# Optimization experiments

Measured on AMD Instinct MI355X. Metric: run time of the kernel, lower is better.

## Reference

```python
import jax, jax.numpy as jnp
import numpy as np

NUM_GRAPHS = 128
NUM_LAYERS = 3
BN_EPS = 1e-5


def setup_inputs() -> dict:
    key = jax.random.key(0)
    ks = jax.random.split(key, 8)
    N, E, D, C = 100000, 1250000, 64, 10
    x = jax.random.normal(ks[0], (N, D), dtype=jnp.float32)
    edge_index = jax.random.randint(ks[1], (2, E), 0, N, dtype=jnp.int64)
    batch = jnp.sort(jax.random.randint(ks[2], (N,), 0, NUM_GRAPHS, dtype=jnp.int64))
    W_rel = jax.random.normal(ks[3], (NUM_LAYERS, D, D), dtype=jnp.float32) * (1.0 / np.sqrt(D))
    b_rel = jax.random.normal(ks[4], (NUM_LAYERS, D), dtype=jnp.float32) * 0.01
    W_root = jax.random.normal(ks[5], (NUM_LAYERS, D, D), dtype=jnp.float32) * (1.0 / np.sqrt(D))
    gamma = jnp.ones((NUM_LAYERS, D), dtype=jnp.float32)
    beta = jnp.zeros((NUM_LAYERS, D), dtype=jnp.float32)
    W_cls = jax.random.normal(ks[6], (D, C), dtype=jnp.float32) * (1.0 / np.sqrt(D))
    b_cls = jnp.zeros((C,), dtype=jnp.float32)
    return {"x": x, "edge_index": edge_index, "batch": batch,
            "W_rel": W_rel, "b_rel": b_rel, "W_root": W_root,
            "gamma": gamma, "beta": beta, "W_cls": W_cls, "b_cls": b_cls}


def reference(x, edge_index, batch, W_rel, b_rel, W_root, gamma, beta, W_cls, b_cls):
    N = x.shape[0]
    src, dst = edge_index[0], edge_index[1]
    for l in range(NUM_LAYERS):
        # GraphConv: lin_rel(sum-aggregated neighbor feats) + lin_root(x)
        msg = jax.ops.segment_sum(x[src], dst, num_segments=N)  # [N, D]
        h = msg @ W_rel[l] + b_rel[l] + x @ W_root[l]
        # BatchNorm1d over nodes (batch statistics, training-mode math)
        mean = jnp.mean(h, axis=0)
        var = jnp.var(h, axis=0)
        h = (h - mean) * jax.lax.rsqrt(var + BN_EPS) * gamma[l] + beta[l]
        x = jax.nn.relu(h)  # dropout is identity at inference
    # global_mean_pool: segment mean over graph ids
    counts = jax.ops.segment_sum(jnp.ones((N,), dtype=x.dtype), batch, num_segments=NUM_GRAPHS)
    pooled = jax.ops.segment_sum(x, batch, num_segments=NUM_GRAPHS)
    pooled = pooled / jnp.maximum(counts, 1.0)[:, None]  # [G, D]
    return pooled @ W_cls + b_cls
```

## Files before the change

### kernel.cpp

```cpp
#include <hip/hip_runtime.h>

#define D 64
#define NGRAPH 128
#define NCLS 10
#define BN_EPS 1e-5f
#define BUCK_SZ 512
#define EPB 8192

typedef __attribute__((ext_vector_type(8))) __bf16 bf16x8;
typedef __attribute__((ext_vector_type(4))) float floatx4;

union BF8 { bf16x8 v; ushort u[8]; };

__device__ __forceinline__ unsigned f2bf_rne(float f) {
  unsigned u = __float_as_uint(f);
  return (u + 0x7FFFu + ((u >> 16) & 1u)) >> 16;
}
__device__ __forceinline__ unsigned pack2bf(float a, float b) {
  return f2bf_rne(a) | (f2bf_rne(b) << 16);
}
__device__ __forceinline__ float4 bf4_to_f4(uint2 u) {
  float4 r;
  r.x = __uint_as_float(u.x << 16);
  r.y = __uint_as_float(u.x & 0xFFFF0000u);
  r.z = __uint_as_float(u.y << 16);
  r.w = __uint_as_float(u.y & 0xFFFF0000u);
  return r;
}

__device__ __forceinline__ void bn_sc_sh(
    const float* __restrict__ stats, const float* __restrict__ gamma,
    const float* __restrict__ beta, float invN, int f, float* sc, float* sh) {
  float mean = stats[f] * invN;
  float var = stats[D + f] * invN - mean * mean;
  float s = gamma[f] * rsqrtf(var + BN_EPS);
  *sc = s;
  *sh = beta[f] - mean * s;
}

__device__ __forceinline__ void split8(float4 a, float4 b,
                                       bf16x8* hi, bf16x8* lo) {
  float f[8] = {a.x, a.y, a.z, a.w, b.x, b.y, b.z, b.w};
  BF8 H, L;
#pragma unroll
  for (int t = 0; t < 8; t++) {
    unsigned u = __float_as_uint(f[t]);
    H.u[t] = (ushort)(u >> 16);
    float hf = __uint_as_float(u & 0xFFFF0000u);
    float lf = f[t] - hf;
    L.u[t] = (ushort)(__float_as_uint(lf) >> 16);
  }
  *hi = H.v;
  *lo = L.v;
}

__global__ __launch_bounds__(256) void bucket_scatter_kernel(
    const int* __restrict__ ei, int* __restrict__ gcnt, int* __restrict__ pk,
    int E, int capB, int nbuck) {
  __shared__ int hist[256];
  __shared__ int base[256];
  int t = threadIdx.x;
  int e0 = blockIdx.x * EPB;
  int e1 = min(e0 + EPB, E);
  hist[t] = 0;
  __syncthreads();
  for (int e = e0 + t; e < e1; e += 256)
    atomicAdd(&hist[ei[E + e] >> 9], 1);
  __syncthreads();
  int h = hist[t];
  if (t < nbuck && h > 0) base[t] = atomicAdd(&gcnt[t], h);
  hist[t] = 0;
  __syncthreads();
  for (int e = e0 + t; e < e1; e += 256) {
    int s = ei[e];
    int d = ei[E + e];
    int b = d >> 9;
    int pos = base[b] + atomicAdd(&hist[b], 1);
    if (pos < capB) pk[(size_t)b * capB + pos] = (s << 9) | (d & (BUCK_SZ - 1));
  }
}

__global__ void bucket_scan_kernel(const int* __restrict__ gcnt,
                                   int* __restrict__ bstart,
                                   int* __restrict__ row_start,
                                   int nbuck, int N, int capB) {
  __shared__ int s[256];
  int t = threadIdx.x;
  int v = (t < nbuck) ? min(gcnt[t], capB) : 0;
  s[t] = v;
  __syncthreads();
  for (int off = 1; off < 256; off <<= 1) {
    int add = (t >= off) ? s[t - off] : 0;
    __syncthreads();
    s[t] += add;
    __syncthreads();
  }
  if (t < nbuck) bstart[t] = s[t] - v;
  if (t == 0) {
    bstart[nbuck] = s[255];
    row_start[N] = s[255];
  }
}

__global__ __launch_bounds__(256) void bucket_place_kernel(
    const int* __restrict__ pk, const int* __restrict__ gcnt,
    const int* __restrict__ bstart, int* __restrict__ row_start,
    int* __restrict__ csr_src, int N, int capB) {
  __shared__ int hist[BUCK_SZ];
  __shared__ int scn[256];
  __shared__ int cur[BUCK_SZ];
  int b = blockIdx.x;
  int t = threadIdx.x;
  hist[t] = 0;
  hist[t + 256] = 0;
  int cnt = min(gcnt[b], capB);
  const int* seg = pk + (size_t)b * capB;
  __syncthreads();
  for (int e = t; e < cnt; e += 256)
    atomicAdd(&hist[seg[e] & (BUCK_SZ - 1)], 1);
  __syncthreads();
  scn[t] = hist[2 * t] + hist[2 * t + 1];
  __syncthreads();
  for (int off = 1; off < 256; off <<= 1) {
    int add = (t >= off) ? scn[t - off] : 0;
    __syncthreads();
    scn[t] += add;
    __syncthreads();
  }
  int base = bstart[b];
  int ex = (t == 0) ? 0 : scn[t - 1];
  int c0 = base + ex;
  int c1 = c0 + hist[2 * t];
  cur[2 * t] = c0;
  cur[2 * t + 1] = c1;
  int dst0 = b * BUCK_SZ + 2 * t;
  if (dst0 < N) row_start[dst0] = c0;
  if (dst0 + 1 < N) row_start[dst0 + 1] = c1;
  __syncthreads();
  for (int e = t; e < cnt; e += 256) {
    int p = seg[e];
    int slot = atomicAdd(&cur[p & (BUCK_SZ - 1)], 1);
    csr_src[slot] = p >> 9;
  }
}

__global__ __launch_bounds__(256) void wsplit_kernel(
    const float* __restrict__ Wrel, const float* __restrict__ Wroot,
    ushort* __restrict__ wfrag) {
  int l = blockIdx.x;
  const float* Wr = Wrel + l * 4096;
  const float* Wo = Wroot + l * 4096;
  ushort* base = wfrag + l * 16384;
  for (int slot = threadIdx.x; slot < 1024; slot += 256) {
    int kt = slot >> 8, nt = (slot >> 6) & 3, lane = slot & 63;
    int quad = lane >> 4, c = lane & 15;
    ushort* ph = base + (((kt * 4 + nt) * 2 + 0) * 64 + lane) * 8;
    ushort* pl = base + (((kt * 4 + nt) * 2 + 1) * 64 + lane) * 8;
#pragma unroll
    for (int j = 0; j < 8; j++) {
      int k = kt * 32 + quad * 8 + j;
      int n = nt * 16 + c;
      float w = (k < 64) ? Wr[k * 64 + n] : Wo[(k - 64) * 64 + n];
      unsigned u = __float_as_uint(w);
      ph[j] = (ushort)(u >> 16);
      float lf = w - __uint_as_float(u & 0xFFFF0000u);
      pl[j] = (ushort)(__float_as_uint(lf) >> 16);
    }
  }
}

__global__ __launch_bounds__(256) void xprep_kernel(
    const float* __restrict__ x, ushort* __restrict__ xbf, int n) {
  int base = (blockIdx.x * 256 + threadIdx.x) * 8;
  if (base >= n) return;
  float4 a = *(const float4*)(x + base);
  float4 b = *(const float4*)(x + base + 4);
  uint4 o;
  o.x = pack2bf(a.x, a.y);
  o.y = pack2bf(a.z, a.w);
  o.z = pack2bf(b.x, b.y);
  o.w = pack2bf(b.z, b.w);
  *(uint4*)(xbf + base) = o;
}

__global__ __launch_bounds__(256) void gather_kernel(
    const ushort* __restrict__ xbf, const int* __restrict__ csr_src,
    const int* __restrict__ row_start, const float* __restrict__ stats_prev,
    const float* __restrict__ gamma, const float* __restrict__ beta,
    float invN, int apply, float* __restrict__ msg, int N) {
  int i = blockIdx.x * 4 + (threadIdx.x >> 6);
  int lane = threadIdx.x & 63;
  int q = lane >> 4;
  int f = (lane & 15) << 2;
  if (i >= N) return;
  int e0 = row_start[i], e1 = row_start[i + 1];
  int cnt = e1 - e0;
  int myidx = csr_src[e0 + lane];
  float4 acc = {0.f, 0.f, 0.f, 0.f};
  float4 sc, sh;
  if (apply) {
    bn_sc_sh(stats_prev, gamma, beta, invN, f + 0, &sc.x, &sh.x);
    bn_sc_sh(stats_prev, gamma, beta, invN, f + 1, &sc.y, &sh.y);
    bn_sc_sh(stats_prev, gamma, beta, invN, f + 2, &sc.z, &sh.z);
    bn_sc_sh(stats_prev, gamma, beta, invN, f + 3, &sc.w, &sh.w);
  }

  int cnt64 = min(cnt, 64);
  for (int base = 0; base < cnt64; base += 16) {
    int j0 = base + q;
    int s0 = __shfl(myidx, j0);
    int s1 = __shfl(myidx, j0 + 4);
    int s2 = __shfl(myidx, j0 + 8);
    int s3 = __shfl(myidx, j0 + 12);
    float m0 = (j0 < cnt) ? 1.f : 0.f;
    float m1 = (j0 + 4 < cnt) ? 1.f : 0.f;
    float m2 = (j0 + 8 < cnt) ? 1.f : 0.f;
    float m3 = (j0 + 12 < cnt) ? 1.f : 0.f;
    s0 = (j0 < cnt) ? s0 : 0;
    s1 = (j0 + 4 < cnt) ? s1 : 0;
    s2 = (j0 + 8 < cnt) ? s2 : 0;
    s3 = (j0 + 12 < cnt) ? s3 : 0;
    float4 v0 = bf4_to_f4(*(const uint2*)(xbf + (size_t)s0 * D + f));
    float4 v1 = bf4_to_f4(*(const uint2*)(xbf + (size_t)s1 * D + f));
    float4 v2 = bf4_to_f4(*(const uint2*)(xbf + (size_t)s2 * D + f));
    float4 v3 = bf4_to_f4(*(const uint2*)(xbf + (size_t)s3 * D + f));
    if (apply) {
      acc.x += m0 * fmaxf(v0.x * sc.x + sh.x, 0.f) + m1 * fmaxf(v1.x * sc.x + sh.x, 0.f)
             + m2 * fmaxf(v2.x * sc.x + sh.x, 0.f) + m3 * fmaxf(v3.x * sc.x + sh.x, 0.f);
      acc.y += m0 * fmaxf(v0.y * sc.y + sh.y, 0.f) + m1 * fmaxf(v1.y * sc.y + sh.y, 0.f)
             + m2 * fmaxf(v2.y * sc.y + sh.y, 0.f) + m3 * fmaxf(v3.y * sc.y + sh.y, 0.f);
      acc.z += m0 * fmaxf(v0.z * sc.z + sh.z, 0.f) + m1 * fmaxf(v1.z * sc.z + sh.z, 0.f)
             + m2 * fmaxf(v2.z * sc.z + sh.z, 0.f) + m3 * fmaxf(v3.z * sc.z + sh.z, 0.f);
      acc.w += m0 * fmaxf(v0.w * sc.w + sh.w, 0.f) + m1 * fmaxf(v1.w * sc.w + sh.w, 0.f)
             + m2 * fmaxf(v2.w * sc.w + sh.w, 0.f) + m3 * fmaxf(v3.w * sc.w + sh.w, 0.f);
    } else {
      acc.x += m0 * v0.x + m1 * v1.x + m2 * v2.x + m3 * v3.x;
      acc.y += m0 * v0.y + m1 * v1.y + m2 * v2.y + m3 * v3.y;
      acc.z += m0 * v0.z + m1 * v1.z + m2 * v2.z + m3 * v3.z;
      acc.w += m0 * v0.w + m1 * v1.w + m2 * v2.w + m3 * v3.w;
    }
  }

  for (int e = e0 + 64 + q; e < e1; e += 4) {
    float4 v = bf4_to_f4(*(const uint2*)(xbf + (size_t)csr_src[e] * D + f));
    if (apply) {
      acc.x += fmaxf(v.x * sc.x + sh.x, 0.f);
      acc.y += fmaxf(v.y * sc.y + sh.y, 0.f);
      acc.z += fmaxf(v.z * sc.z + sh.z, 0.f);
      acc.w += fmaxf(v.w * sc.w + sh.w, 0.f);
    } else {
      acc.x += v.x; acc.y += v.y; acc.z += v.z; acc.w += v.w;
    }
  }

  acc.x += __shfl_xor(acc.x, 16); acc.x += __shfl_xor(acc.x, 32);
  acc.y += __shfl_xor(acc.y, 16); acc.y += __shfl_xor(acc.y, 32);
  acc.z += __shfl_xor(acc.z, 16); acc.z += __shfl_xor(acc.z, 32);
  acc.w += __shfl_xor(acc.w, 16); acc.w += __shfl_xor(acc.w, 32);
  if (q == 0) *(float4*)(msg + (size_t)i * D + f) = acc;
}

__global__ __launch_bounds__(256, 1) void mm_mfma_kernel(
    const float* msg, const float* xf32, const ushort* xbfin,
    const ushort* __restrict__ wfrag, const float* __restrict__ brel,
    const float* __restrict__ stats_prev, const float* __restrict__ gamma,
    const float* __restrict__ beta, float invN, int apply,
    float* h, ushort* hbf, int wh, int wbf, float* __restrict__ stats_cur,
    int N, int ntiles, int nwaves) {
  __shared__ float ssum[4][64];
  __shared__ float ssq[4][64];
  int tid = threadIdx.x;
  int lane = tid & 63;
  int wvid = tid >> 6;
  int wv = (blockIdx.x * 256 + tid) >> 6;
  int quad = lane >> 4;
  int lo4 = lane & 15;

  bf16x8 bf[4][4][2];
#pragma unroll
  for (int kt = 0; kt < 4; kt++)
#pragma unroll
    for (int nt = 0; nt < 4; nt++)
#pragma unroll
      for (int s = 0; s < 2; s++)
        bf[kt][nt][s] =
            *(const bf16x8*)(wfrag + (((kt * 4 + nt) * 2 + s) * 64 + lane) * 8);

  float bias[4];
#pragma unroll
  for (int nt = 0; nt < 4; nt++) bias[nt] = brel[nt * 16 + lo4];

  float scx[2][8], shx[2][8];
  if (apply) {
#pragma unroll
    for (int hh = 0; hh < 2; hh++)
#pragma unroll
      for (int jj = 0; jj < 8; jj++) {
        int f = hh * 32 + quad * 8 + jj;
        bn_sc_sh(stats_prev, gamma, beta, invN, f, &scx[hh][jj], &shx[hh][jj]);
      }
  }

  float psum[4] = {0.f, 0.f, 0.f, 0.f};
  float psq[4] = {0.f, 0.f, 0.f, 0.f};

  for (int t = wv; t < ntiles; t += nwaves) {
    int i0 = t * 16;
    int row = i0 + lo4;
    if (row >= N) row = N - 1;
    bf16x8 ahi[4], alo[4];
#pragma unroll
    for (int kt = 0; kt < 4; kt++) {
      float4 a, b;
      if (kt < 2) {
        const float* p = msg + (size_t)row * D + (kt & 1) * 32 + quad * 8;
        a = *(const float4*)p;
        b = *(const float4*)(p + 4);
      } else if (apply) {
        const ushort* p = xbfin + (size_t)row * D + (kt & 1) * 32 + quad * 8;
        uint4 u = *(const uint4*)p;
        uint2 ulo = {u.x, u.y}, uhi = {u.z, u.w};
        a = bf4_to_f4(ulo);
        b = bf4_to_f4(uhi);
        int hh = kt - 2;
        a.x = fmaxf(a.x * scx[hh][0] + shx[hh][0], 0.f);
        a.y = fmaxf(a.y * scx[hh][1] + shx[hh][1], 0.f);
        a.z = fmaxf(a.z * scx[hh][2] + shx[hh][2], 0.f);
        a.w = fmaxf(a.w * scx[hh][3] + shx[hh][3], 0.f);
        b.x = fmaxf(b.x * scx[hh][4] + shx[hh][4], 0.f);
        b.y = fmaxf(b.y * scx[hh][5] + shx[hh][5], 0.f);
        b.z = fmaxf(b.z * scx[hh][6] + shx[hh][6], 0.f);
        b.w = fmaxf(b.w * scx[hh][7] + shx[hh][7], 0.f);
      } else {
        const float* p = xf32 + (size_t)row * D + (kt & 1) * 32 + quad * 8;
        a = *(const float4*)p;
        b = *(const float4*)(p + 4);
      }
      split8(a, b, &ahi[kt], &alo[kt]);
    }
#pragma unroll
    for (int nt = 0; nt < 4; nt++) {
      floatx4 acc = {bias[nt], bias[nt], bias[nt], bias[nt]};
#pragma unroll
      for (int kt = 0; kt < 4; kt++) {
        acc = __builtin_amdgcn_mfma_f32_16x16x32_bf16(ahi[kt], bf[kt][nt][0],
                                                      acc, 0, 0, 0);
        acc = __builtin_amdgcn_mfma_f32_16x16x32_bf16(ahi[kt], bf[kt][nt][1],
                                                      acc, 0, 0, 0);
        acc = __builtin_amdgcn_mfma_f32_16x16x32_bf16(alo[kt], bf[kt][nt][0],
                                                      acc, 0, 0, 0);
      }
#pragma unroll
      for (int r = 0; r < 4; r++) {
        int grow = i0 + quad * 4 + r;
        if (grow < N) {
          float v = acc[r];
          size_t idx = (size_t)grow * D + nt * 16 + lo4;
          if (wh) h[idx] = v;
          if (wbf) hbf[idx] = (ushort)f2bf_rne(v);
          psum[nt] += v;
          psq[nt] += v * v;
        }
      }
    }
  }

#pragma unroll
  for (int nt = 0; nt < 4; nt++) {
    float s = psum[nt], q = psq[nt];
    s += __shfl_xor(s, 16); s += __shfl_xor(s, 32);
    q += __shfl_xor(q, 16); q += __shfl_xor(q, 32);
    if (lane < 16) { ssum[wvid][nt * 16 + lane] = s; ssq[wvid][nt * 16 + lane] = q; }
  }
  __syncthreads();
  if (tid < 64) {
    atomicAdd(&stats_cur[tid],
              ssum[0][tid] + ssum[1][tid] + ssum[2][tid] + ssum[3][tid]);
  } else if (tid < 128) {
    int c = tid - 64;
    atomicAdd(&stats_cur[D + c],
              ssq[0][c] + ssq[1][c] + ssq[2][c] + ssq[3][c]);
  }
}

__global__ __launch_bounds__(256) void norm_relu_pool_kernel(
    const float* __restrict__ h, const float* __restrict__ stats,
    const float* __restrict__ gamma, const float* __restrict__ beta,
    float invN, const int* __restrict__ batch, float* __restrict__ pooled,
    int N) {
  int j = threadIdx.x & 63;
  int q = threadIdx.x >> 6;
  int i0 = blockIdx.x * 256;
  float sc, sh;
  bn_sc_sh(stats, gamma, beta, invN, j, &sc, &sh);
  int curg = -1;
  float acc = 0.f;
  for (int r = q; r < 256; r += 4) {
    int i = i0 + r;
    if (i >= N) break;
    int b = batch[i];
    float v = fmaxf(h[(size_t)i * D + j] * sc + sh, 0.f);
    if (b != curg) {
      if (curg >= 0) atomicAdd(&pooled[curg * D + j], acc);
      curg = b;
      acc = v;
    } else {
      acc += v;
    }
  }
  if (curg >= 0) atomicAdd(&pooled[curg * D + j], acc);
}

__global__ void cls_kernel(const float* __restrict__ pooled,
                           const int* __restrict__ batch,
                           const float* __restrict__ Wcls,
                           const float* __restrict__ bcls,
                           float* __restrict__ out, int N) {
  int tid = blockIdx.x * blockDim.x + threadIdx.x;
  if (tid >= NGRAPH * NCLS) return;
  int g = tid / NCLS, c = tid % NCLS;
  int lo = 0, hi = N;
  while (lo < hi) { int m = (lo + hi) >> 1; if (batch[m] < g) lo = m + 1; else hi = m; }
  int start = lo;
  lo = 0; hi = N;
  while (lo < hi) { int m = (lo + hi) >> 1; if (batch[m] <= g) lo = m + 1; else hi = m; }
  float inv = 1.f / fmaxf((float)(lo - start), 1.f);
  float acc = bcls[c];
#pragma unroll 8
  for (int k = 0; k < D; k++) acc += pooled[g * D + k] * inv * Wcls[k * NCLS + c];
  out[g * NCLS + c] = acc;
}

extern "C" void kernel_launch(void* const* d_in, const int* in_sizes, int n_in,
                              void* d_out, int out_size, void* d_ws, size_t ws_size,
                              hipStream_t stream) {
  const float* x      = (const float*)d_in[0];
  const int*   ei     = (const int*)d_in[1];
  const int*   batch  = (const int*)d_in[2];
  const float* W_rel  = (const float*)d_in[3];
  const float* b_rel  = (const float*)d_in[4];
  const float* W_root = (const float*)d_in[5];
  const float* gamma  = (const float*)d_in[6];
  const float* beta   = (const float*)d_in[7];
  const float* W_cls  = (const float*)d_in[8];
  const float* b_cls  = (const float*)d_in[9];
  float* out = (float*)d_out;

  int E = in_sizes[1] / 2;
  int N = in_sizes[2];
  size_t nd = (size_t)N * D;
  int nbuck = (N + BUCK_SZ - 1) / BUCK_SZ;
  int capB = ((2 * E / nbuck) + 511) & ~511;
  if (capB < 1024) capB = 1024;
  float invN = 1.0f / (float)N;

  float* bufA    = (float*)d_ws;
  float* bufB    = bufA + nd;
  ushort* xbf    = (ushort*)(bufB + nd);
  float* stats3  = (float*)(xbf + nd);
  float* pooled  = stats3 + 3 * 2 * D;
  int* gcnt      = (int*)(pooled + NGRAPH * D);
  ushort* wfrag  = (ushort*)(gcnt + ((nbuck + 3) & ~3));
  int* bstart    = (int*)(wfrag + 3 * 16384);
  int* row_start = bstart + nbuck + 1;
  int* csr_src   = row_start + N + 1;
  int* pk        = csr_src + E;

  size_t zero_bytes = (size_t)(3 * 2 * D + NGRAPH * D) * 4 +
                      (size_t)nbuck * 4;
  hipMemsetAsync(stats3, 0, zero_bytes, stream);

  bucket_scatter_kernel<<<(E + EPB - 1) / EPB, 256, 0, stream>>>(
      ei, gcnt, pk, E, capB, nbuck);
  bucket_scan_kernel<<<1, 256, 0, stream>>>(gcnt, bstart, row_start, nbuck, N, capB);
  bucket_place_kernel<<<nbuck, 256, 0, stream>>>(pk, gcnt, bstart, row_start,
                                                 csr_src, N, capB);
  wsplit_kernel<<<3, 256, 0, stream>>>(W_rel, W_root, wfrag);
  xprep_kernel<<<(int)((nd / 8 + 255) / 256), 256, 0, stream>>>(x, xbf, (int)nd);

  const int MM_BLOCKS = 512;
  const int MM_WAVES = MM_BLOCKS * 4;
  int ntiles = (N + 15) / 16;
  for (int l = 0; l < 3; l++) {
    int apply = (l > 0) ? 1 : 0;
    int wbf = (l < 2) ? 1 : 0;
    int wh = (l == 2) ? 1 : 0;
    const float* st_prev = stats3 + (l > 0 ? (l - 1) * 2 * D : 0);
    const float* gm_prev = gamma + (l > 0 ? (l - 1) * D : 0);
    const float* bt_prev = beta + (l > 0 ? (l - 1) * D : 0);
    float* st_cur = stats3 + l * 2 * D;

    gather_kernel<<<(N + 3) / 4, 256, 0, stream>>>(
        xbf, csr_src, row_start, st_prev, gm_prev, bt_prev, invN, apply,
        bufB, N);

    mm_mfma_kernel<<<MM_BLOCKS, 256, 0, stream>>>(
        bufB, x, xbf, wfrag + l * 16384, b_rel + l * D,
        st_prev, gm_prev, bt_prev, invN, apply,
        bufA, xbf , wh, wbf, st_cur,
        N, ntiles, MM_WAVES);
  }

  norm_relu_pool_kernel<<<(N + 255) / 256, 256, 0, stream>>>(
      bufA, stats3 + 2 * 2 * D, gamma + 2 * D, beta + 2 * D, invN, batch,
      pooled, N);
  cls_kernel<<<(NGRAPH * NCLS + 255) / 256, 256, 0, stream>>>(
      pooled, batch, W_cls, b_cls, out, N);
}
```

Measured before the change: 357.9 us.

## Materialize normalized bf16 activations once instead of re-normalizing per gathered edge

Adds a separate norm_kernel that applies BatchNorm and ReLU to the raw bf16 layer output once per node, writing a normalized bf16 buffer with a zero padding row. The gather and matmul kernels then read pre-normalized values, so the per-edge scale, shift and ReLU and the per-thread BN parameter setup go away. Masked lanes now point at the zero row instead of using multiplicative masks. The cost is an extra kernel launch and an extra read and write pass over N×64 bf16 values per layer.

```diff
diff --git a/kernel.cpp b/kernel.cpp
--- a/kernel.cpp
+++ b/kernel.cpp
@@ -170,24 +170,57 @@
 }
 
 __global__ __launch_bounds__(256) void xprep_kernel(
-    const float* __restrict__ x, ushort* __restrict__ xbf, int n) {
+    const float* __restrict__ x, ushort* __restrict__ xbf, int n, int ntot) {
   int base = (blockIdx.x * 256 + threadIdx.x) * 8;
-  if (base >= n) return;
-  float4 a = *(const float4*)(x + base);
-  float4 b = *(const float4*)(x + base + 4);
-  uint4 o;
-  o.x = pack2bf(a.x, a.y);
-  o.y = pack2bf(a.z, a.w);
-  o.z = pack2bf(b.x, b.y);
-  o.w = pack2bf(b.z, b.w);
+  if (base >= ntot) return;
+  uint4 o = {0, 0, 0, 0};
+  if (base < n) {
+    float4 a = *(const float4*)(x + base);
+    float4 b = *(const float4*)(x + base + 4);
+    o.x = pack2bf(a.x, a.y);
+    o.y = pack2bf(a.z, a.w);
+    o.z = pack2bf(b.x, b.y);
+    o.w = pack2bf(b.z, b.w);
+  }
   *(uint4*)(xbf + base) = o;
+}
+
+__global__ __launch_bounds__(256) void norm_kernel(
+    const ushort* __restrict__ hraw, const float* __restrict__ stats,
+    const float* __restrict__ gamma, const float* __restrict__ beta,
+    float invN, ushort* __restrict__ xnorm, int n, int ntot) {
+  int base = (blockIdx.x * 256 + threadIdx.x) * 8;
+  if (base >= ntot) return;
+  uint4 o = {0, 0, 0, 0};
+  if (base < n) {
+    int f0 = base & 63;
+    uint4 u = *(const uint4*)(hraw + base);
+    uint2 ulo = {u.x, u.y}, uhi = {u.z, u.w};
+    float4 a = bf4_to_f4(ulo);
+    float4 b = bf4_to_f4(uhi);
+    float sc[8], sh[8];
+#pragma unroll
+    for (int k = 0; k < 8; k++)
+      bn_sc_sh(stats, gamma, beta, invN, f0 + k, &sc[k], &sh[k]);
+    a.x = fmaxf(a.x * sc[0] + sh[0], 0.f);
+    a.y = fmaxf(a.y * sc[1] + sh[1], 0.f);
+    a.z = fmaxf(a.z * sc[2] + sh[2], 0.f);
+    a.w = fmaxf(a.w * sc[3] + sh[3], 0.f);
+    b.x = fmaxf(b.x * sc[4] + sh[4], 0.f);
+    b.y = fmaxf(b.y * sc[5] + sh[5], 0.f);
+    b.z = fmaxf(b.z * sc[6] + sh[6], 0.f);
+    b.w = fmaxf(b.w * sc[7] + sh[7], 0.f);
+    o.x = pack2bf(a.x, a.y);
+    o.y = pack2bf(a.z, a.w);
+    o.z = pack2bf(b.x, b.y);
+    o.w = pack2bf(b.z, b.w);
+  }
+  *(uint4*)(xnorm + base) = o;
 }
 
 __global__ __launch_bounds__(256) void gather_kernel(
     const ushort* __restrict__ xbf, const int* __restrict__ csr_src,
-    const int* __restrict__ row_start, const float* __restrict__ stats_prev,
-    const float* __restrict__ gamma, const float* __restrict__ beta,
-    float invN, int apply, float* __restrict__ msg, int N) {
+    const int* __restrict__ row_start, float* __restrict__ msg, int N) {
   int i = blockIdx.x * 4 + (threadIdx.x >> 6);
   int lane = threadIdx.x & 63;
   int q = lane >> 4;
@@ -197,13 +230,6 @@
   int cnt = e1 - e0;
   int myidx = csr_src[e0 + lane];
   float4 acc = {0.f, 0.f, 0.f, 0.f};
-  float4 sc, sh;
-  if (apply) {
-    bn_sc_sh(stats_prev, gamma, beta, invN, f + 0, &sc.x, &sh.x);
-    bn_sc_sh(stats_prev, gamma, beta, invN, f + 1, &sc.y, &sh.y);
-    bn_sc_sh(stats_prev, gamma, beta, invN, f + 2, &sc.z, &sh.z);
-    bn_sc_sh(stats_prev, gamma, beta, invN, f + 3, &sc.w, &sh.w);
-  }
 
   int cnt64 = min(cnt, 64);
   for (int base = 0; base < cnt64; base += 16) {
@@ -212,45 +238,23 @@
     int s1 = __shfl(myidx, j0 + 4);
     int s2 = __shfl(myidx, j0 + 8);
     int s3 = __shfl(myidx, j0 + 12);
-    float m0 = (j0 < cnt) ? 1.f : 0.f;
-    float m1 = (j0 + 4 < cnt) ? 1.f : 0.f;
-    float m2 = (j0 + 8 < cnt) ? 1.f : 0.f;
-    float m3 = (j0 + 12 < cnt) ? 1.f : 0.f;
-    s0 = (j0 < cnt) ? s0 : 0;
-    s1 = (j0 + 4 < cnt) ? s1 : 0;
-    s2 = (j0 + 8 < cnt) ? s2 : 0;
-    s3 = (j0 + 12 < cnt) ? s3 : 0;
+    s0 = (j0 < cnt) ? s0 : N;
+    s1 = (j0 + 4 < cnt) ? s1 : N;
+    s2 = (j0 + 8 < cnt) ? s2 : N;
+    s3 = (j0 + 12 < cnt) ? s3 : N;
     float4 v0 = bf4_to_f4(*(const uint2*)(xbf + (size_t)s0 * D + f));
     float4 v1 = bf4_to_f4(*(const uint2*)(xbf + (size_t)s1 * D + f));
     float4 v2 = bf4_to_f4(*(const uint2*)(xbf + (size_t)s2 * D + f));
     float4 v3 = bf4_to_f4(*(const uint2*)(xbf + (size_t)s3 * D + f));
-    if (apply) {
-      acc.x += m0 * fmaxf(v0.x * sc.x + sh.x, 0.f) + m1 * fmaxf(v1.x * sc.x + sh.x, 0.f)
-             + m2 * fmaxf(v2.x * sc.x + sh.x, 0.f) + m3 * fmaxf(v3.x * sc.x + sh.x, 0.f);
-      acc.y += m0 * fmaxf(v0.y * sc.y + sh.y, 0.f) + m1 * fmaxf(v1.y * sc.y + sh.y, 0.f)
-             + m2 * fmaxf(v2.y * sc.y + sh.y, 0.f) + m3 * fmaxf(v3.y * sc.y + sh.y, 0.f);
-      acc.z += m0 * fmaxf(v0.z * sc.z + sh.z, 0.f) + m1 * fmaxf(v1.z * sc.z + sh.z, 0.f)
-             + m2 * fmaxf(v2.z * sc.z + sh.z, 0.f) + m3 * fmaxf(v3.z * sc.z + sh.z, 0.f);
-      acc.w += m0 * fmaxf(v0.w * sc.w + sh.w, 0.f) + m1 * fmaxf(v1.w * sc.w + sh.w, 0.f)
-             + m2 * fmaxf(v2.w * sc.w + sh.w, 0.f) + m3 * fmaxf(v3.w * sc.w + sh.w, 0.f);
-    } else {
-      acc.x += m0 * v0.x + m1 * v1.x + m2 * v2.x + m3 * v3.x;
-      acc.y += m0 * v0.y + m1 * v1.y + m2 * v2.y + m3 * v3.y;
-      acc.z += m0 * v0.z + m1 * v1.z + m2 * v2.z + m3 * v3.z;
-      acc.w += m0 * v0.w + m1 * v1.w + m2 * v2.w + m3 * v3.w;
-    }
+    acc.x += (v0.x + v1.x) + (v2.x + v3.x);
+    acc.y += (v0.y + v1.y) + (v2.y + v3.y);
+    acc.z += (v0.z + v1.z) + (v2.z + v3.z);
+    acc.w += (v0.w + v1.w) + (v2.w + v3.w);
   }
 
   for (int e = e0 + 64 + q; e < e1; e += 4) {
     float4 v = bf4_to_f4(*(const uint2*)(xbf + (size_t)csr_src[e] * D + f));
-    if (apply) {
-      acc.x += fmaxf(v.x * sc.x + sh.x, 0.f);
-      acc.y += fmaxf(v.y * sc.y + sh.y, 0.f);
-      acc.z += fmaxf(v.z * sc.z + sh.z, 0.f);
-      acc.w += fmaxf(v.w * sc.w + sh.w, 0.f);
-    } else {
-      acc.x += v.x; acc.y += v.y; acc.z += v.z; acc.w += v.w;
-    }
+    acc.x += v.x; acc.y += v.y; acc.z += v.z; acc.w += v.w;
   }
 
   acc.x += __shfl_xor(acc.x, 16); acc.x += __shfl_xor(acc.x, 32);
@@ -261,11 +265,11 @@
 }
 
 __global__ __launch_bounds__(256, 1) void mm_mfma_kernel(
-    const float* msg, const float* xf32, const ushort* xbfin,
+    const float* __restrict__ msg, const float* __restrict__ xf32,
+    const ushort* __restrict__ xbfin,
     const ushort* __restrict__ wfrag, const float* __restrict__ brel,
-    const float* __restrict__ stats_prev, const float* __restrict__ gamma,
-    const float* __restrict__ beta, float invN, int apply,
-    float* h, ushort* hbf, int wh, int wbf, float* __restrict__ stats_cur,
+    int use_bf, float* __restrict__ h, ushort* __restrict__ hbf,
+    int wh, int wbf, float* __restrict__ stats_cur,
     int N, int ntiles, int nwaves) {
   __shared__ float ssum[4][64];
   __shared__ float ssq[4][64];
@@ -290,17 +294,6 @@
 #pragma unroll
   for (int nt = 0; nt < 4; nt++) bias[nt] = brel[nt * 16 + lo4];
 
-  float scx[2][8], shx[2][8];
-  if (apply) {
-#pragma unroll
-    for (int hh = 0; hh < 2; hh++)
-#pragma unroll
-      for (int jj = 0; jj < 8; jj++) {
-        int f = hh * 32 + quad * 8 + jj;
-        bn_sc_sh(stats_prev, gamma, beta, invN, f, &scx[hh][jj], &shx[hh][jj]);
-      }
-  }
-
   float psum[4] = {0.f, 0.f, 0.f, 0.f};
   float psq[4] = {0.f, 0.f, 0.f, 0.f};
 
@@ -316,21 +309,12 @@
         const float* p = msg + (size_t)row * D + (kt & 1) * 32 + quad * 8;
         a = *(const float4*)p;
         b = *(const float4*)(p + 4);
-      } else if (apply) {
+      } else if (use_bf) {
         const ushort* p = xbfin + (size_t)row * D + (kt & 1) * 32 + quad * 8;
         uint4 u = *(const uint4*)p;
         uint2 ulo = {u.x, u.y}, uhi = {u.z, u.w};
         a = bf4_to_f4(ulo);
         b = bf4_to_f4(uhi);
-        int hh = kt - 2;
-        a.x = fmaxf(a.x * scx[hh][0] + shx[hh][0], 0.f);
-        a.y = fmaxf(a.y * scx[hh][1] + shx[hh][1], 0.f);
-        a.z = fmaxf(a.z * scx[hh][2] + shx[hh][2], 0.f);
-        a.w = fmaxf(a.w * scx[hh][3] + shx[hh][3], 0.f);
-        b.x = fmaxf(b.x * scx[hh][4] + shx[hh][4], 0.f);
-        b.y = fmaxf(b.y * scx[hh][5] + shx[hh][5], 0.f);
-        b.z = fmaxf(b.z * scx[hh][6] + shx[hh][6], 0.f);
-        b.w = fmaxf(b.w * scx[hh][7] + shx[hh][7], 0.f);
       } else {
         const float* p = xf32 + (size_t)row * D + (kt & 1) * 32 + quad * 8;
         a = *(const float4*)p;
@@ -449,6 +433,7 @@
   int E = in_sizes[1] / 2;
   int N = in_sizes[2];
   size_t nd = (size_t)N * D;
+  size_t ndp = (size_t)(N + 1) * D;
   int nbuck = (N + BUCK_SZ - 1) / BUCK_SZ;
   int capB = ((2 * E / nbuck) + 511) & ~511;
   if (capB < 1024) capB = 1024;
@@ -456,8 +441,9 @@
 
   float* bufA    = (float*)d_ws;
   float* bufB    = bufA + nd;
-  ushort* xbf    = (ushort*)(bufB + nd);
-  float* stats3  = (float*)(xbf + nd);
+  ushort* xnorm  = (ushort*)(bufB + nd);
+  ushort* hraw   = xnorm + ndp;
+  float* stats3  = (float*)(hraw + nd);
   float* pooled  = stats3 + 3 * 2 * D;
   int* gcnt      = (int*)(pooled + NGRAPH * D);
   ushort* wfrag  = (ushort*)(gcnt + ((nbuck + 3) & ~3));
@@ -476,29 +462,32 @@
   bucket_place_kernel<<<nbuck, 256, 0, stream>>>(pk, gcnt, bstart, row_start,
                                                  csr_src, N, capB);
   wsplit_kernel<<<3, 256, 0, stream>>>(W_rel, W_root, wfrag);
-  xprep_kernel<<<(int)((nd / 8 + 255) / 256), 256, 0, stream>>>(x, xbf, (int)nd);
+  xprep_kernel<<<(int)((ndp / 8 + 255) / 256), 256, 0, stream>>>(
+      x, xnorm, (int)nd, (int)ndp);
 
   const int MM_BLOCKS = 512;
   const int MM_WAVES = MM_BLOCKS * 4;
   int ntiles = (N + 15) / 16;
+  int nblk_norm = (int)((ndp / 8 + 255) / 256);
   for (int l = 0; l < 3; l++) {
-    int apply = (l > 0) ? 1 : 0;
+    int use_bf = (l > 0) ? 1 : 0;
     int wbf = (l < 2) ? 1 : 0;
     int wh = (l == 2) ? 1 : 0;
-    const float* st_prev = stats3 + (l > 0 ? (l - 1) * 2 * D : 0);
-    const float* gm_prev = gamma + (l > 0 ? (l - 1) * D : 0);
-    const float* bt_prev = beta + (l > 0 ? (l - 1) * D : 0);
     float* st_cur = stats3 + l * 2 * D;
 
-    gather_kernel<<<(N + 3) / 4, 256, 0, stream>>>(
-        xbf, csr_src, row_start, st_prev, gm_prev, bt_prev, invN, apply,
-        bufB, N);
+    gather_kernel<<<(N + 3) / 4, 256, 0, stream>>>(xnorm, csr_src, row_start,
+                                                   bufB, N);
 
     mm_mfma_kernel<<<MM_BLOCKS, 256, 0, stream>>>(
-        bufB, x, xbf, wfrag + l * 16384, b_rel + l * D,
-        st_prev, gm_prev, bt_prev, invN, apply,
-        bufA, xbf , wh, wbf, st_cur,
+        bufB, x, xnorm, wfrag + l * 16384, b_rel + l * D,
+        use_bf, bufA, hraw, wh, wbf, st_cur,
         N, ntiles, MM_WAVES);
+
+    if (l < 2) {
+      norm_kernel<<<nblk_norm, 256, 0, stream>>>(
+          hraw, st_cur, gamma + l * D, beta + l * D, invN, xnorm,
+          (int)nd, (int)ndp);
+    }
   }
 
   norm_relu_pool_kernel<<<(N + 255) / 256, 256, 0, stream>>>(
```

After: 358.1 us. About the same (+0.0%).
